# Kernel tuning notes

Hardware: AMD Instinct MI355X
Metric: run time of the kernel (lower is better)

Reference implementation:

```python
import math
import jax, jax.numpy as jnp
import numpy as np

N_HEADS = 16


def setup_inputs() -> dict:
    key = jax.random.key(0)
    k1, k2 = jax.random.split(key)
    N, H, C, T = 2, N_HEADS, 64, 2048
    qkv = jax.random.normal(k1, (N, H * 3 * C, T), dtype=jnp.float32)
    mask = jax.random.randint(k2, (N, 1, T), 0, 2).astype(bool) | (jnp.arange(T)[None, None, :] < T // 2)
    return {"qkv": qkv, "mask": mask}


def reference(qkv, mask):
    bs, width, length = qkv.shape
    ch = width // (3 * N_HEADS)
    qkv_r = qkv.reshape(bs * N_HEADS, 3 * ch, length)
    q, k, v = qkv_r[:, :ch], qkv_r[:, ch:2 * ch], qkv_r[:, 2 * ch:]
    scale = 1.0 / math.sqrt(math.sqrt(ch))
    # [bH, T, T] scores in float32 (matches weight.float())
    weight = jnp.einsum('bct,bcs->bts', q * scale, k * scale).astype(jnp.float32)
    inv = ~mask[:, 0, :]                                   # [N, T] True = pad
    m = inv[:, None, :] | inv[:, :, None]                  # [N, T, T]
    m = jnp.broadcast_to(m[:, None], (bs, N_HEADS, length, length)).reshape(-1, length, length)
    weight = jnp.where(m, jnp.finfo(weight.dtype).min, weight)
    weight = jax.nn.softmax(weight, axis=-1)
    a = jnp.einsum('bts,bcs->bct', weight, v)              # [bH, C, T]
    return a.reshape(bs, -1, length)
```

## Files before the change

### kernel.cpp

```cpp
#include <hip/hip_runtime.h>
#include <hip/hip_bf16.h>
#include <stdint.h>

namespace {

constexpr int T_LEN = 2048;
constexpr int NROWS = 192;
constexpr int QBLK  = 64;
constexpr int NBH   = 32;
constexpr int KT_STRIDE = 72;
constexpr int TILE_ELEMS = 64 * KT_STRIDE;
constexpr int TILE_BYTES = TILE_ELEMS * 2;

typedef float f32x4 __attribute__((ext_vector_type(4)));
typedef short bf16x8 __attribute__((ext_vector_type(8)));
typedef short bf16x4 __attribute__((ext_vector_type(4)));

__device__ __forceinline__ unsigned short f2bf(float f) {
  union { float f; unsigned u; } v; v.f = f;
  unsigned r = v.u + 0x7fffu + ((v.u >> 16) & 1u);
  return (unsigned short)(r >> 16);
}
__device__ __forceinline__ unsigned pack2(float a, float b) {
  return (unsigned)f2bf(a) | ((unsigned)f2bf(b) << 16);
}
__device__ __forceinline__ float fast_exp2(float x) {
#if __has_builtin(__builtin_amdgcn_exp2f)
  return __builtin_amdgcn_exp2f(x);
#else
  return exp2f(x);
#endif
}
__device__ __forceinline__ f32x4 mfma_16x16x16_bf16(bf16x4 a, bf16x4 b, f32x4 c) {
#if __has_builtin(__builtin_amdgcn_mfma_f32_16x16x16bf16_1k)
  return __builtin_amdgcn_mfma_f32_16x16x16bf16_1k(a, b, c, 0, 0, 0);
#else
  asm("v_mfma_f32_16x16x16_bf16 %0, %1, %2, %0" : "+v"(c) : "v"(a), "v"(b));
  return c;
#endif
}
__device__ __forceinline__ void gload_lds16(const void* g, void* l) {
  __builtin_amdgcn_global_load_lds(
      (const __attribute__((address_space(1))) unsigned int*)g,
      (__attribute__((address_space(3))) unsigned int*)l, 16, 0, 0);
}

}

__global__ void nm_kernel(const unsigned char* __restrict__ raw,
                          unsigned char* __restrict__ outm, int n) {
  int stride = (raw[1] != 0) ? 1 : ((raw[4] != 0) ? 4 : 8);
  int i = blockIdx.x * blockDim.x + threadIdx.x;
  if (i < n) outm[i] = (raw[(size_t)i * stride] != 0) ? 1 : 0;
}

__global__ void bias9_kernel(const unsigned char* __restrict__ raw,
                             float* __restrict__ bias, int n) {
  int stride = (raw[1] != 0) ? 1 : ((raw[4] != 0) ? 4 : 8);
  int i = blockIdx.x * blockDim.x + threadIdx.x;
  if (i < n) bias[i] = (raw[(size_t)i * stride] != 0) ? 0.0f : -1.0e30f;
  else if (i < n + T_LEN) bias[i] = 0.0f;
}


__global__ __launch_bounds__(256) void tq9_kernel(const float* __restrict__ qkv,
                                                  const unsigned char* __restrict__ mraw,
                                                  short* __restrict__ qtg,
                                                  short* __restrict__ ktg) {
  __shared__ float tile[64][65];
  const int t = threadIdx.x;
  const int which = blockIdx.z;
  const int bh = blockIdx.y;
  const int bx = blockIdx.x;
  const int s0 = bx * 64;
  const float* src = qkv + (size_t)bh * NROWS * T_LEN + (size_t)which * 64 * T_LEN;
  const int c = t >> 2;
  #pragma unroll
  for (int p = 0; p < 4; ++p) {
    int col = (t & 3) * 4 + p * 16;
    float4 v = *(const float4*)&src[(size_t)c * T_LEN + s0 + col];
    tile[c][col] = v.x; tile[c][col + 1] = v.y;
    tile[c][col + 2] = v.z; tile[c][col + 3] = v.w;
  }
  __syncthreads();
  const int s = t & 63;
  float scale;
  if (which) {
    scale = 1.0f;
  } else {
    const int mstride = (mraw[1] != 0) ? 1 : ((mraw[4] != 0) ? 4 : 8);
    const int nb = bh >> 4;
    const bool live = mraw[((size_t)nb * T_LEN + s0 + s) * mstride] != 0;
    scale = live ? 0.18033688011112042f : 0.0f;
  }
  #pragma unroll
  for (int p = 0; p < 2; ++p) {
    int jc = (t >> 6) * 2 + p;
    bf16x4 o0, o1;
    #pragma unroll
    for (int i = 0; i < 4; ++i) {
      o0[i] = (short)f2bf(tile[jc * 8 + i][s] * scale);
      o1[i] = (short)f2bf(tile[jc * 8 + 4 + i][s] * scale);
    }
    short* d = which
      ? (ktg + (size_t)(bh * 32 + bx) * TILE_ELEMS + s * KT_STRIDE + jc * 8)
      : (qtg + (size_t)bh * T_LEN * 64 + (size_t)(s0 + s) * 64 + jc * 8);
    *(bf16x4*)d = o0;
    *(bf16x4*)(d + 4) = o1;
  }
}

__global__ __launch_bounds__(256) void cv3_kernel(const float* __restrict__ qkv,
                                                  short* __restrict__ vtg) {
  int cid = blockIdx.x * 256 + threadIdx.x;
  int bh = cid >> 14;
  int rem = cid & 16383;
  int c = rem >> 8;
  int cg = rem & 255;
  int grp = cg >> 3, jin = cg & 7;
  const float* src = qkv + (size_t)bh * NROWS * T_LEN + (size_t)(128 + c) * T_LEN + cg * 8;
  float4 a = *(const float4*)src;
  float4 b = *(const float4*)(src + 4);
  bf16x4 o0, o1;
  o0[0] = (short)f2bf(a.x); o0[1] = (short)f2bf(a.y);
  o0[2] = (short)f2bf(a.z); o0[3] = (short)f2bf(a.w);
  o1[0] = (short)f2bf(b.x); o1[1] = (short)f2bf(b.y);
  o1[2] = (short)f2bf(b.z); o1[3] = (short)f2bf(b.w);
  short* d = vtg + (size_t)(bh * 32 + grp) * TILE_ELEMS + c * KT_STRIDE + jin * 8;
  *(bf16x4*)d = o0;
  *(bf16x4*)(d + 4) = o1;
}


__global__ __launch_bounds__(512, 4) void attn11_kernel(const short* __restrict__ qtg,
                                                        const short* __restrict__ ktg,
                                                        const short* __restrict__ vtg,
                                                        const float* __restrict__ bias,
                                                        int mask_elems,
                                                        float* __restrict__ out) {
  __shared__ __align__(16) short smem[4 * TILE_ELEMS];

  const int tid  = threadIdx.x;
  const int lane = tid & 63;
  const int wv   = tid >> 6;
  const int sgrp = wv & 3;
  const int tgrp = wv >> 2;
  const int l15  = lane & 15;
  const int g    = lane >> 4;

  int id = blockIdx.x;
  id = (id & 7) * 128 + (id >> 3);
  const int bh = id >> 5;
  const int t0 = (id & 31) * QBLK;
  const int nb = bh >> 4;

  const int tA = t0 + (tgrp * 2) * 16 + l15;
  const int tB = tA + 16;

  const short* Qbase = qtg + (size_t)bh * T_LEN * 64;
  const bf16x8 qfA0 = *(const bf16x8*)(Qbase + (size_t)tA * 64 + g * 8);
  const bf16x8 qfA1 = *(const bf16x8*)(Qbase + (size_t)tA * 64 + 32 + g * 8);
  const bf16x8 qfB0 = *(const bf16x8*)(Qbase + (size_t)tB * 64 + g * 8);
  const bf16x8 qfB1 = *(const bf16x8*)(Qbase + (size_t)tB * 64 + 32 + g * 8);

  const float btA = bias[(size_t)nb * T_LEN + tA];
  const float btB = bias[(size_t)nb * T_LEN + tB];
  const float* __restrict__ browA = bias + ((btA != 0.0f) ? (size_t)mask_elems
                                                          : (size_t)nb * T_LEN);
  const float* __restrict__ browB = bias + ((btB != 0.0f) ? (size_t)mask_elems
                                                          : (size_t)nb * T_LEN);

  const char* __restrict__ kt0 = (const char*)(ktg + (size_t)bh * 32 * TILE_ELEMS);
  const char* __restrict__ vt0 = (const char*)(vtg + (size_t)bh * 32 * TILE_ELEMS);
  char* KtL = (char*)smem;
  char* VsL = (char*)(smem + 2 * TILE_ELEMS);

  gload_lds16(kt0 + wv * 1024 + lane * 16, KtL + wv * 1024);
  gload_lds16(vt0 + wv * 1024 + lane * 16, VsL + wv * 1024);
  if (wv == 0) gload_lds16(kt0 + 8192 + lane * 16, KtL + 8192);
  if (wv == 1) gload_lds16(vt0 + 8192 + lane * 16, VsL + 8192);
  __syncthreads();

  f32x4 accA[4], accB[4];
  #pragma unroll
  for (int i = 0; i < 4; ++i) { accA[i] = (f32x4){0.f,0.f,0.f,0.f}; accB[i] = accA[i]; }
  float lA = 0.0f, lB = 0.0f;

  const int koff = (sgrp * 16 + l15) * KT_STRIDE;
  const int boff = sgrp * 16 + g * 4;

  int cur = 0;
  for (int sb = 0; sb < T_LEN / 64; ++sb) {
    if (sb + 1 < T_LEN / 64) {
      const char* ks = kt0 + (size_t)(sb + 1) * TILE_BYTES;
      const char* vs = vt0 + (size_t)(sb + 1) * TILE_BYTES;
      char* Ktn = KtL + (cur ^ 1) * TILE_BYTES;
      char* Vsn = VsL + (cur ^ 1) * TILE_BYTES;
      gload_lds16(ks + wv * 1024 + lane * 16, Ktn + wv * 1024);
      gload_lds16(vs + wv * 1024 + lane * 16, Vsn + wv * 1024);
      if (wv == 0) gload_lds16(ks + 8192 + lane * 16, Ktn + 8192);
      if (wv == 1) gload_lds16(vs + 8192 + lane * 16, Vsn + 8192);
    }

    const short* Ktc = smem + cur * TILE_ELEMS;
    const short* Vsc = smem + (2 + cur) * TILE_ELEMS;

    bf16x8 kf0 = *(const bf16x8*)&Ktc[koff + g * 8];
    bf16x8 kf1 = *(const bf16x8*)&Ktc[koff + 32 + g * 8];

    f32x4 SA = (f32x4){0.f, 0.f, 0.f, 0.f};
    SA = __builtin_amdgcn_mfma_f32_16x16x32_bf16(kf0, qfA0, SA, 0, 0, 0);
    SA = __builtin_amdgcn_mfma_f32_16x16x32_bf16(kf1, qfA1, SA, 0, 0, 0);
    f32x4 SB = (f32x4){0.f, 0.f, 0.f, 0.f};
    SB = __builtin_amdgcn_mfma_f32_16x16x32_bf16(kf0, qfB0, SB, 0, 0, 0);
    SB = __builtin_amdgcn_mfma_f32_16x16x32_bf16(kf1, qfB1, SB, 0, 0, 0);

    const f32x4 b4A = *(const f32x4*)&browA[sb * 64 + boff];
    const f32x4 b4B = *(const f32x4*)&browB[sb * 64 + boff];
    float pA0 = fast_exp2(SA[0] + b4A[0]);
    float pA1 = fast_exp2(SA[1] + b4A[1]);
    float pA2 = fast_exp2(SA[2] + b4A[2]);
    float pA3 = fast_exp2(SA[3] + b4A[3]);
    lA += (pA0 + pA1) + (pA2 + pA3);
    float pB0 = fast_exp2(SB[0] + b4B[0]);
    float pB1 = fast_exp2(SB[1] + b4B[1]);
    float pB2 = fast_exp2(SB[2] + b4B[2]);
    float pB3 = fast_exp2(SB[3] + b4B[3]);
    lB += (pB0 + pB1) + (pB2 + pB3);

    union { bf16x4 v; __hip_bfloat162 h[2]; } pfA, pfB;
    pfA.h[0] = __float22bfloat162_rn(float2{pA0, pA1});
    pfA.h[1] = __float22bfloat162_rn(float2{pA2, pA3});
    pfB.h[0] = __float22bfloat162_rn(float2{pB0, pB1});
    pfB.h[1] = __float22bfloat162_rn(float2{pB2, pB3});

    #pragma unroll
    for (int cb = 0; cb < 4; ++cb) {
      bf16x4 vf = *(const bf16x4*)&Vsc[(cb * 16 + l15) * KT_STRIDE + sgrp * 16 + g * 4];
      accA[cb] = mfma_16x16x16_bf16(vf, pfA.v, accA[cb]);
      accB[cb] = mfma_16x16x16_bf16(vf, pfB.v, accB[cb]);
    }

    __syncthreads();
    cur ^= 1;
  }

  float* scr = (float*)smem;
  {
    const int lb = lane * 36;
    if (sgrp >= 2) {
      float* base = scr + ((sgrp - 2) * 2 + tgrp) * 2304 + lb;
      #pragma unroll
      for (int cb = 0; cb < 4; ++cb) {
        *(f32x4*)&base[cb * 4] = accA[cb];
        *(f32x4*)&base[16 + cb * 4] = accB[cb];
      }
      base[32] = lA; base[33] = lB;
    }
    __syncthreads();
    if (sgrp < 2) {
      const float* base = scr + (sgrp * 2 + tgrp) * 2304 + lb;
      #pragma unroll
      for (int cb = 0; cb < 4; ++cb) {
        accA[cb] += *(const f32x4*)&base[cb * 4];
        accB[cb] += *(const f32x4*)&base[16 + cb * 4];
      }
      lA += base[32]; lB += base[33];
    }
    __syncthreads();
    if (sgrp == 1) {
      float* base = scr + tgrp * 2304 + lb;
      #pragma unroll
      for (int cb = 0; cb < 4; ++cb) {
        *(f32x4*)&base[cb * 4] = accA[cb];
        *(f32x4*)&base[16 + cb * 4] = accB[cb];
      }
      base[32] = lA; base[33] = lB;
    }
    __syncthreads();
    if (sgrp == 0) {
      const float* base = scr + tgrp * 2304 + lb;
      #pragma unroll
      for (int cb = 0; cb < 4; ++cb) {
        accA[cb] += *(const f32x4*)&base[cb * 4];
        accB[cb] += *(const f32x4*)&base[16 + cb * 4];
      }
      lA += base[32]; lB += base[33];

      lA += __shfl_xor(lA, 16, 64);
      lA += __shfl_xor(lA, 32, 64);
      lB += __shfl_xor(lB, 16, 64);
      lB += __shfl_xor(lB, 32, 64);
      const float ilA = 1.0f / lA;
      const float ilB = 1.0f / lB;
      const size_t out_base = (size_t)bh * 64 * T_LEN;
      #pragma unroll
      for (int cb = 0; cb < 4; ++cb) {
        #pragma unroll
        for (int r = 0; r < 4; ++r) {
          int c = cb * 16 + g * 4 + r;
          out[out_base + (size_t)c * T_LEN + tA] = accA[cb][r] * ilA;
          out[out_base + (size_t)c * T_LEN + tB] = accB[cb][r] * ilB;
        }
      }
    }
  }
}


__global__ __launch_bounds__(256) void attn_fb_kernel(const float* __restrict__ qkv,
                                                      const unsigned char* __restrict__ maskn,
                                                      float* __restrict__ out) {
  __shared__ __align__(16) short Kt[QBLK * KT_STRIDE];
  __shared__ __align__(16) short Vs[64 * KT_STRIDE];
  __shared__ __align__(16) unsigned char Ms[T_LEN];

  const int tid  = threadIdx.x;
  const int lane = tid & 63;
  const int wv   = tid >> 6;
  const int l15  = lane & 15;
  const int g    = lane >> 4;

  const int bh = blockIdx.y;
  const int nb = bh >> 4;
  const int t0 = blockIdx.x * QBLK;

  const float* __restrict__ Qg = qkv + (size_t)bh * NROWS * T_LEN;
  const float* __restrict__ Kg = Qg + (size_t)64 * T_LEN;
  const float* __restrict__ Vg = Qg + (size_t)128 * T_LEN;

  {
    const uint2* src = (const uint2*)(maskn + (size_t)nb * T_LEN);
    ((uint2*)Ms)[tid] = src[tid];
  }
  {
    const int c2 = (tid >> 6) * 2;
    const int s  = tid & 63;
    #pragma unroll
    for (int p = 0; p < 8; ++p) {
      int c = p * 8 + c2;
      float f0 = Qg[(size_t)c * T_LEN + t0 + s] * 0.125f;
      float f1 = Qg[(size_t)(c + 1) * T_LEN + t0 + s] * 0.125f;
      *(unsigned*)&Kt[s * KT_STRIDE + c] = pack2(f0, f1);
    }
  }
  __syncthreads();

  bf16x8 qf0 = *(const bf16x8*)&Kt[(wv * 16 + l15) * KT_STRIDE + g * 8];
  bf16x8 qf1 = *(const bf16x8*)&Kt[(wv * 16 + l15) * KT_STRIDE + 32 + g * 8];
  const int t_lane = t0 + wv * 16 + l15;
  const bool invt = (Ms[t_lane] == 0);

  f32x4 acc[4];
  #pragma unroll
  for (int i = 0; i < 4; ++i) acc[i] = (f32x4){0.f, 0.f, 0.f, 0.f};
  float m_run = -3.0e38f;
  float l_run = 0.0f;

  for (int sb = 0; sb < T_LEN / 64; ++sb) {
    const int s0 = sb * 64;
    __syncthreads();
    {
      const int c2 = (tid >> 6) * 2;
      const int s  = tid & 63;
      #pragma unroll
      for (int p = 0; p < 8; ++p) {
        int c = p * 8 + c2;
        float f0 = Kg[(size_t)c * T_LEN + s0 + s];
        float f1 = Kg[(size_t)(c + 1) * T_LEN + s0 + s];
        *(unsigned*)&Kt[s * KT_STRIDE + c] = pack2(f0, f1);
      }
    }
    {
      const int cv = (tid >> 5);
      const int s2 = tid & 31;
      #pragma unroll
      for (int p = 0; p < 8; ++p) {
        int c = p * 8 + cv;
        float2 f = *(const float2*)&Vg[(size_t)c * T_LEN + s0 + 2 * s2];
        *(unsigned*)&Vs[c * KT_STRIDE + 2 * s2] = pack2(f.x, f.y);
      }
    }
    __syncthreads();

    #pragma unroll
    for (int st = 0; st < 4; ++st) {
      const int srow = st * 16 + l15;
      bf16x8 kf0 = *(const bf16x8*)&Kt[srow * KT_STRIDE + g * 8];
      bf16x8 kf1 = *(const bf16x8*)&Kt[srow * KT_STRIDE + 32 + g * 8];
      f32x4 S = (f32x4){0.f, 0.f, 0.f, 0.f};
      S = __builtin_amdgcn_mfma_f32_16x16x32_bf16(kf0, qf0, S, 0, 0, 0);
      S = __builtin_amdgcn_mfma_f32_16x16x32_bf16(kf1, qf1, S, 0, 0, 0);

      const unsigned m4 = *(const unsigned*)&Ms[s0 + st * 16 + g * 4];
      float vals[4];
      #pragma unroll
      for (int r = 0; r < 4; ++r) {
        float x = ((m4 >> (8 * r)) & 0xffu) ? S[r] : -1.0e30f;
        vals[r] = invt ? 0.0f : x;
      }
      float pm = fmaxf(fmaxf(vals[0], vals[1]), fmaxf(vals[2], vals[3]));
      pm = fmaxf(pm, __shfl_xor(pm, 16, 64));
      pm = fmaxf(pm, __shfl_xor(pm, 32, 64));
      const float newm = fmaxf(m_run, pm);
      const float alpha = fast_exp2((m_run - newm) * 1.44269504f);
      float p0 = fast_exp2((vals[0] - newm) * 1.44269504f);
      float p1 = fast_exp2((vals[1] - newm) * 1.44269504f);
      float p2 = fast_exp2((vals[2] - newm) * 1.44269504f);
      float p3 = fast_exp2((vals[3] - newm) * 1.44269504f);
      float ps = (p0 + p1) + (p2 + p3);
      ps += __shfl_xor(ps, 16, 64);
      ps += __shfl_xor(ps, 32, 64);
      l_run = l_run * alpha + ps;
      m_run = newm;
      if (__any(alpha < 1.0f)) {
        #pragma unroll
        for (int cb = 0; cb < 4; ++cb)
          #pragma unroll
          for (int r = 0; r < 4; ++r) acc[cb][r] *= alpha;
      }
      bf16x4 pf;
      pf[0] = (short)f2bf(p0); pf[1] = (short)f2bf(p1);
      pf[2] = (short)f2bf(p2); pf[3] = (short)f2bf(p3);
      #pragma unroll
      for (int cb = 0; cb < 4; ++cb) {
        bf16x4 vf = *(const bf16x4*)&Vs[(cb * 16 + l15) * KT_STRIDE + st * 16 + g * 4];
        acc[cb] = mfma_16x16x16_bf16(vf, pf, acc[cb]);
      }
    }
  }

  const float il = 1.0f / l_run;
  const size_t out_base = (size_t)bh * 64 * T_LEN;
  #pragma unroll
  for (int cb = 0; cb < 4; ++cb) {
    #pragma unroll
    for (int r = 0; r < 4; ++r) {
      int c = cb * 16 + g * 4 + r;
      out[out_base + (size_t)c * T_LEN + t_lane] = acc[cb][r] * il;
    }
  }
}


extern "C" void kernel_launch(void* const* d_in, const int* in_sizes, int n_in,
                              void* d_out, int out_size, void* d_ws, size_t ws_size,
                              hipStream_t stream) {
  (void)n_in; (void)out_size;
  const float* qkv = (const float*)d_in[0];
  const unsigned char* mraw = (const unsigned char*)d_in[1];
  float* out = (float*)d_out;
  const int mask_elems = in_sizes[1];

  const size_t QSZ = (size_t)NBH * T_LEN * 64 * sizeof(short);
  const size_t TSZ = (size_t)NBH * 32 * TILE_ELEMS * sizeof(short);
  const size_t BSZ = (size_t)(mask_elems + T_LEN) * sizeof(float);
  const size_t need = QSZ + 2 * TSZ + BSZ;
  if (ws_size >= need) {
    short* qtg = (short*)d_ws;
    short* ktg = (short*)((char*)d_ws + QSZ);
    short* vtg = (short*)((char*)d_ws + QSZ + TSZ);
    float* bias = (float*)((char*)d_ws + QSZ + 2 * TSZ);
    bias9_kernel<<<(mask_elems + T_LEN + 255) / 256, 256, 0, stream>>>(mraw, bias, mask_elems);
    tq9_kernel<<<dim3(T_LEN / 64, NBH, 2), 256, 0, stream>>>(qkv, mraw, qtg, ktg);
    cv3_kernel<<<(NBH * 64 * 256) / 256, 256, 0, stream>>>(qkv, vtg);
    attn11_kernel<<<dim3(NBH * 32), 512, 0, stream>>>(qtg, ktg, vtg, bias, mask_elems, out);
  } else {
    unsigned char* maskn = (unsigned char*)d_ws;
    nm_kernel<<<(mask_elems + 255) / 256, 256, 0, stream>>>(mraw, maskn, mask_elems);
    attn_fb_kernel<<<dim3(T_LEN / QBLK, NBH), 256, 0, stream>>>(qkv, maskn, out);
  }
}
```

Baseline: 92.14 us.

## Fuse prep kernels and double attention query block to 128 with 1024-thread blocks

Merges the bias, Q/K transpose and V conversion kernels into one prep launch, cutting launch overhead. The attention kernel now processes 128 query rows per block with 16 waves, so each K/V tile loaded into LDS serves twice as many queries, and the final cross-wave reduction becomes a serial chain. It also adds s_setprio around the MFMA sections. Risks include fewer blocks (512), launch_bounds(1024,8) register pressure, and a longer reduction tail.

```diff
diff --git a/kernel.cpp b/kernel.cpp
--- a/kernel.cpp
+++ b/kernel.cpp
@@ -6,7 +6,7 @@
 
 constexpr int T_LEN = 2048;
 constexpr int NROWS = 192;
-constexpr int QBLK  = 64;
+constexpr int QBLK  = 128;
 constexpr int NBH   = 32;
 constexpr int KT_STRIDE = 72;
 constexpr int TILE_ELEMS = 64 * KT_STRIDE;
@@ -54,26 +54,48 @@
   if (i < n) outm[i] = (raw[(size_t)i * stride] != 0) ? 1 : 0;
 }
 
-__global__ void bias9_kernel(const unsigned char* __restrict__ raw,
-                             float* __restrict__ bias, int n) {
-  int stride = (raw[1] != 0) ? 1 : ((raw[4] != 0) ? 4 : 8);
-  int i = blockIdx.x * blockDim.x + threadIdx.x;
-  if (i < n) bias[i] = (raw[(size_t)i * stride] != 0) ? 0.0f : -1.0e30f;
-  else if (i < n + T_LEN) bias[i] = 0.0f;
-}
-
-
-__global__ __launch_bounds__(256) void tq9_kernel(const float* __restrict__ qkv,
-                                                  const unsigned char* __restrict__ mraw,
-                                                  short* __restrict__ qtg,
-                                                  short* __restrict__ ktg) {
-  __shared__ float tile[64][65];
-  const int t = threadIdx.x;
-  const int which = blockIdx.z;
+__global__ __launch_bounds__(256) void prep12_kernel(const float* __restrict__ qkv,
+                                                     const unsigned char* __restrict__ mraw,
+                                                     short* __restrict__ qtg,
+                                                     short* __restrict__ ktg,
+                                                     short* __restrict__ vtg,
+                                                     float* __restrict__ bias,
+                                                     int mask_elems) {
+  const int z  = blockIdx.z;
   const int bh = blockIdx.y;
   const int bx = blockIdx.x;
+  const int t  = threadIdx.x;
+
+  if (z >= 2) {
+    int cid = ((bh * 64) + (z - 2) * 32 + bx) * 256 + t;
+    int bh2 = cid >> 14;
+    int rem = cid & 16383;
+    int c = rem >> 8;
+    int cg = rem & 255;
+    int grp = cg >> 3, jin = cg & 7;
+    const float* src = qkv + (size_t)bh2 * NROWS * T_LEN + (size_t)(128 + c) * T_LEN + cg * 8;
+    float4 a = *(const float4*)src;
+    float4 b = *(const float4*)(src + 4);
+    bf16x4 o0, o1;
+    o0[0] = (short)f2bf(a.x); o0[1] = (short)f2bf(a.y);
+    o0[2] = (short)f2bf(a.z); o0[3] = (short)f2bf(a.w);
+    o1[0] = (short)f2bf(b.x); o1[1] = (short)f2bf(b.y);
+    o1[2] = (short)f2bf(b.z); o1[3] = (short)f2bf(b.w);
+    short* d = vtg + (size_t)(bh2 * 32 + grp) * TILE_ELEMS + c * KT_STRIDE + jin * 8;
+    *(bf16x4*)d = o0;
+    *(bf16x4*)(d + 4) = o1;
+    if (z == 2 && bh == 0 && bx < 24) {
+      int i = bx * 256 + t;
+      int stride = (mraw[1] != 0) ? 1 : ((mraw[4] != 0) ? 4 : 8);
+      if (i < mask_elems) bias[i] = (mraw[(size_t)i * stride] != 0) ? 0.0f : -1.0e30f;
+      else if (i < mask_elems + T_LEN) bias[i] = 0.0f;
+    }
+    return;
+  }
+
+  __shared__ float tile[64][65];
   const int s0 = bx * 64;
-  const float* src = qkv + (size_t)bh * NROWS * T_LEN + (size_t)which * 64 * T_LEN;
+  const float* src = qkv + (size_t)bh * NROWS * T_LEN + (size_t)z * 64 * T_LEN;
   const int c = t >> 2;
   #pragma unroll
   for (int p = 0; p < 4; ++p) {
@@ -85,7 +107,7 @@
   __syncthreads();
   const int s = t & 63;
   float scale;
-  if (which) {
+  if (z) {
     scale = 1.0f;
   } else {
     const int mstride = (mraw[1] != 0) ? 1 : ((mraw[4] != 0) ? 4 : 8);
@@ -102,7 +124,7 @@
       o0[i] = (short)f2bf(tile[jc * 8 + i][s] * scale);
       o1[i] = (short)f2bf(tile[jc * 8 + 4 + i][s] * scale);
     }
-    short* d = which
+    short* d = z
       ? (ktg + (size_t)(bh * 32 + bx) * TILE_ELEMS + s * KT_STRIDE + jc * 8)
       : (qtg + (size_t)bh * T_LEN * 64 + (size_t)(s0 + s) * 64 + jc * 8);
     *(bf16x4*)d = o0;
@@ -110,34 +132,13 @@
   }
 }
 
-__global__ __launch_bounds__(256) void cv3_kernel(const float* __restrict__ qkv,
-                                                  short* __restrict__ vtg) {
-  int cid = blockIdx.x * 256 + threadIdx.x;
-  int bh = cid >> 14;
-  int rem = cid & 16383;
-  int c = rem >> 8;
-  int cg = rem & 255;
-  int grp = cg >> 3, jin = cg & 7;
-  const float* src = qkv + (size_t)bh * NROWS * T_LEN + (size_t)(128 + c) * T_LEN + cg * 8;
-  float4 a = *(const float4*)src;
-  float4 b = *(const float4*)(src + 4);
-  bf16x4 o0, o1;
-  o0[0] = (short)f2bf(a.x); o0[1] = (short)f2bf(a.y);
-  o0[2] = (short)f2bf(a.z); o0[3] = (short)f2bf(a.w);
-  o1[0] = (short)f2bf(b.x); o1[1] = (short)f2bf(b.y);
-  o1[2] = (short)f2bf(b.z); o1[3] = (short)f2bf(b.w);
-  short* d = vtg + (size_t)(bh * 32 + grp) * TILE_ELEMS + c * KT_STRIDE + jin * 8;
-  *(bf16x4*)d = o0;
-  *(bf16x4*)(d + 4) = o1;
-}
-
-
-__global__ __launch_bounds__(512, 4) void attn11_kernel(const short* __restrict__ qtg,
-                                                        const short* __restrict__ ktg,
-                                                        const short* __restrict__ vtg,
-                                                        const float* __restrict__ bias,
-                                                        int mask_elems,
-                                                        float* __restrict__ out) {
+
+__global__ __launch_bounds__(1024, 8) void attn12_kernel(const short* __restrict__ qtg,
+                                                         const short* __restrict__ ktg,
+                                                         const short* __restrict__ vtg,
+                                                         const float* __restrict__ bias,
+                                                         int mask_elems,
+                                                         float* __restrict__ out) {
   __shared__ __align__(16) short smem[4 * TILE_ELEMS];
 
   const int tid  = threadIdx.x;
@@ -149,12 +150,12 @@
   const int g    = lane >> 4;
 
   int id = blockIdx.x;
-  id = (id & 7) * 128 + (id >> 3);
-  const int bh = id >> 5;
-  const int t0 = (id & 31) * QBLK;
+  id = (id & 7) * 64 + (id >> 3);
+  const int bh = id >> 4;
+  const int t0 = (id & 15) * QBLK;
   const int nb = bh >> 4;
 
-  const int tA = t0 + (tgrp * 2) * 16 + l15;
+  const int tA = t0 + tgrp * 32 + l15;
   const int tB = tA + 16;
 
   const short* Qbase = qtg + (size_t)bh * T_LEN * 64;
@@ -175,10 +176,11 @@
   char* KtL = (char*)smem;
   char* VsL = (char*)(smem + 2 * TILE_ELEMS);
 
-  gload_lds16(kt0 + wv * 1024 + lane * 16, KtL + wv * 1024);
-  gload_lds16(vt0 + wv * 1024 + lane * 16, VsL + wv * 1024);
-  if (wv == 0) gload_lds16(kt0 + 8192 + lane * 16, KtL + 8192);
-  if (wv == 1) gload_lds16(vt0 + 8192 + lane * 16, VsL + 8192);
+  {
+    if (wv < 9)  gload_lds16(kt0 + wv * 1024 + lane * 16, KtL + wv * 1024);
+    if (wv >= 9) gload_lds16(vt0 + (wv - 9) * 1024 + lane * 16, VsL + (wv - 9) * 1024);
+    if (wv < 2)  gload_lds16(vt0 + (7 + wv) * 1024 + lane * 16, VsL + (7 + wv) * 1024);
+  }
   __syncthreads();
 
   f32x4 accA[4], accB[4];
@@ -196,10 +198,9 @@
       const char* vs = vt0 + (size_t)(sb + 1) * TILE_BYTES;
       char* Ktn = KtL + (cur ^ 1) * TILE_BYTES;
       char* Vsn = VsL + (cur ^ 1) * TILE_BYTES;
-      gload_lds16(ks + wv * 1024 + lane * 16, Ktn + wv * 1024);
-      gload_lds16(vs + wv * 1024 + lane * 16, Vsn + wv * 1024);
-      if (wv == 0) gload_lds16(ks + 8192 + lane * 16, Ktn + 8192);
-      if (wv == 1) gload_lds16(vs + 8192 + lane * 16, Vsn + 8192);
+      if (wv < 9)  gload_lds16(ks + wv * 1024 + lane * 16, Ktn + wv * 1024);
+      if (wv >= 9) gload_lds16(vs + (wv - 9) * 1024 + lane * 16, Vsn + (wv - 9) * 1024);
+      if (wv < 2)  gload_lds16(vs + (7 + wv) * 1024 + lane * 16, Vsn + (7 + wv) * 1024);
     }
 
     const short* Ktc = smem + cur * TILE_ELEMS;
@@ -208,12 +209,14 @@
     bf16x8 kf0 = *(const bf16x8*)&Ktc[koff + g * 8];
     bf16x8 kf1 = *(const bf16x8*)&Ktc[koff + 32 + g * 8];
 
+    __builtin_amdgcn_s_setprio(1);
     f32x4 SA = (f32x4){0.f, 0.f, 0.f, 0.f};
     SA = __builtin_amdgcn_mfma_f32_16x16x32_bf16(kf0, qfA0, SA, 0, 0, 0);
     SA = __builtin_amdgcn_mfma_f32_16x16x32_bf16(kf1, qfA1, SA, 0, 0, 0);
     f32x4 SB = (f32x4){0.f, 0.f, 0.f, 0.f};
     SB = __builtin_amdgcn_mfma_f32_16x16x32_bf16(kf0, qfB0, SB, 0, 0, 0);
     SB = __builtin_amdgcn_mfma_f32_16x16x32_bf16(kf1, qfB1, SB, 0, 0, 0);
+    __builtin_amdgcn_s_setprio(0);
 
     const f32x4 b4A = *(const f32x4*)&browA[sb * 64 + boff];
     const f32x4 b4B = *(const f32x4*)&browB[sb * 64 + boff];
@@ -234,84 +237,68 @@
     pfB.h[0] = __float22bfloat162_rn(float2{pB0, pB1});
     pfB.h[1] = __float22bfloat162_rn(float2{pB2, pB3});
 
+    __builtin_amdgcn_s_setprio(1);
     #pragma unroll
     for (int cb = 0; cb < 4; ++cb) {
       bf16x4 vf = *(const bf16x4*)&Vsc[(cb * 16 + l15) * KT_STRIDE + sgrp * 16 + g * 4];
       accA[cb] = mfma_16x16x16_bf16(vf, pfA.v, accA[cb]);
       accB[cb] = mfma_16x16x16_bf16(vf, pfB.v, accB[cb]);
     }
+    __builtin_amdgcn_s_setprio(0);
 
     __syncthreads();
     cur ^= 1;
   }
 
   float* scr = (float*)smem;
-  {
-    const int lb = lane * 36;
-    if (sgrp >= 2) {
-      float* base = scr + ((sgrp - 2) * 2 + tgrp) * 2304 + lb;
+  const int lb = tgrp * 2304 + lane * 36;
+  #define DUMP_ROW  { float* b_ = scr + lb;                                   \
+      _Pragma("unroll") for (int cb = 0; cb < 4; ++cb) {                      \
+        *(f32x4*)&b_[cb * 4] = accA[cb]; *(f32x4*)&b_[16 + cb * 4] = accB[cb];} \
+      b_[32] = lA; b_[33] = lB; }
+  #define ADD_ROW   { const float* b_ = scr + lb;                             \
+      _Pragma("unroll") for (int cb = 0; cb < 4; ++cb) {                      \
+        accA[cb] += *(const f32x4*)&b_[cb * 4];                               \
+        accB[cb] += *(const f32x4*)&b_[16 + cb * 4]; }                        \
+      lA += b_[32]; lB += b_[33]; }
+  if (sgrp == 3) DUMP_ROW
+  __syncthreads();
+  if (sgrp == 1) ADD_ROW
+  __syncthreads();
+  if (sgrp == 2) DUMP_ROW
+  __syncthreads();
+  if (sgrp == 0) ADD_ROW
+  __syncthreads();
+  if (sgrp == 1) DUMP_ROW
+  __syncthreads();
+  if (sgrp == 0) {
+    ADD_ROW
+    lA += __shfl_xor(lA, 16, 64);
+    lA += __shfl_xor(lA, 32, 64);
+    lB += __shfl_xor(lB, 16, 64);
+    lB += __shfl_xor(lB, 32, 64);
+    const float ilA = 1.0f / lA;
+    const float ilB = 1.0f / lB;
+    const size_t out_base = (size_t)bh * 64 * T_LEN;
+    #pragma unroll
+    for (int cb = 0; cb < 4; ++cb) {
       #pragma unroll
-      for (int cb = 0; cb < 4; ++cb) {
-        *(f32x4*)&base[cb * 4] = accA[cb];
-        *(f32x4*)&base[16 + cb * 4] = accB[cb];
-      }
-      base[32] = lA; base[33] = lB;
-    }
-    __syncthreads();
-    if (sgrp < 2) {
-      const float* base = scr + (sgrp * 2 + tgrp) * 2304 + lb;
-      #pragma unroll
-      for (int cb = 0; cb < 4; ++cb) {
-        accA[cb] += *(const f32x4*)&base[cb * 4];
-        accB[cb] += *(const f32x4*)&base[16 + cb * 4];
-      }
-      lA += base[32]; lB += base[33];
-    }
-    __syncthreads();
-    if (sgrp == 1) {
-      float* base = scr + tgrp * 2304 + lb;
-      #pragma unroll
-      for (int cb = 0; cb < 4; ++cb) {
-        *(f32x4*)&base[cb * 4] = accA[cb];
-        *(f32x4*)&base[16 + cb * 4] = accB[cb];
-      }
-      base[32] = lA; base[33] = lB;
-    }
-    __syncthreads();
-    if (sgrp == 0) {
-      const float* base = scr + tgrp * 2304 + lb;
-      #pragma unroll
-      for (int cb = 0; cb < 4; ++cb) {
-        accA[cb] += *(const f32x4*)&base[cb * 4];
-        accB[cb] += *(const f32x4*)&base[16 + cb * 4];
-      }
-      lA += base[32]; lB += base[33];
-
-      lA += __shfl_xor(lA, 16, 64);
-      lA += __shfl_xor(lA, 32, 64);
-      lB += __shfl_xor(lB, 16, 64);
-      lB += __shfl_xor(lB, 32, 64);
-      const float ilA = 1.0f / lA;
-      const float ilB = 1.0f / lB;
-      const size_t out_base = (size_t)bh * 64 * T_LEN;
-      #pragma unroll
-      for (int cb = 0; cb < 4; ++cb) {
-        #pragma unroll
-        for (int r = 0; r < 4; ++r) {
-          int c = cb * 16 + g * 4 + r;
-          out[out_base + (size_t)c * T_LEN + tA] = accA[cb][r] * ilA;
-          out[out_base + (size_t)c * T_LEN + tB] = accB[cb][r] * ilB;
-        }
-      }
-    }
-  }
+      for (int r = 0; r < 4; ++r) {
+        int c = cb * 16 + g * 4 + r;
+        out[out_base + (size_t)c * T_LEN + tA] = accA[cb][r] * ilA;
+        out[out_base + (size_t)c * T_LEN + tB] = accB[cb][r] * ilB;
+      }
+    }
+  }
+  #undef DUMP_ROW
+  #undef ADD_ROW
 }
 
 
 __global__ __launch_bounds__(256) void attn_fb_kernel(const float* __restrict__ qkv,
                                                       const unsigned char* __restrict__ maskn,
                                                       float* __restrict__ out) {
-  __shared__ __align__(16) short Kt[QBLK * KT_STRIDE];
+  __shared__ __align__(16) short Kt[64 * KT_STRIDE];
   __shared__ __align__(16) short Vs[64 * KT_STRIDE];
   __shared__ __align__(16) unsigned char Ms[T_LEN];
 
@@ -323,7 +310,7 @@
 
   const int bh = blockIdx.y;
   const int nb = bh >> 4;
-  const int t0 = blockIdx.x * QBLK;
+  const int t0 = blockIdx.x * 64;
 
   const float* __restrict__ Qg = qkv + (size_t)bh * NROWS * T_LEN;
   const float* __restrict__ Kg = Qg + (size_t)64 * T_LEN;
@@ -461,13 +448,13 @@
     short* ktg = (short*)((char*)d_ws + QSZ);
     short* vtg = (short*)((char*)d_ws + QSZ + TSZ);
     float* bias = (float*)((char*)d_ws + QSZ + 2 * TSZ);
-    bias9_kernel<<<(mask_elems + T_LEN + 255) / 256, 256, 0, stream>>>(mraw, bias, mask_elems);
-    tq9_kernel<<<dim3(T_LEN / 64, NBH, 2), 256, 0, stream>>>(qkv, mraw, qtg, ktg);
-    cv3_kernel<<<(NBH * 64 * 256) / 256, 256, 0, stream>>>(qkv, vtg);
-    attn11_kernel<<<dim3(NBH * 32), 512, 0, stream>>>(qtg, ktg, vtg, bias, mask_elems, out);
+    prep12_kernel<<<dim3(32, NBH, 4), 256, 0, stream>>>(qkv, mraw, qtg, ktg, vtg,
+                                                        bias, mask_elems);
+    attn12_kernel<<<dim3(NBH * 16), 1024, 0, stream>>>(qtg, ktg, vtg, bias,
+                                                       mask_elems, out);
   } else {
     unsigned char* maskn = (unsigned char*)d_ws;
     nm_kernel<<<(mask_elems + 255) / 256, 256, 0, stream>>>(mraw, maskn, mask_elems);
-    attn_fb_kernel<<<dim3(T_LEN / QBLK, NBH), 256, 0, stream>>>(qkv, maskn, out);
-  }
-}
+    attn_fb_kernel<<<dim3(T_LEN / 64, NBH), 256, 0, stream>>>(qkv, maskn, out);
+  }
+}
```

Result: slower. 211.7 us (+129.7%).
